# Performance work log

Measured on AMD Instinct MI355X. Metric: run time of the kernel, lower is better.

The kernel has to match this reference:

```python
import jax, jax.numpy as jnp
import numpy as np

B, T, C = 4, 2048, 1024
NH = 16
HD = C // NH


def setup_inputs() -> dict:
    key = jax.random.key(0)
    k1, k2, k3 = jax.random.split(key, 3)
    x = jax.random.normal(k1, (B, T, C), dtype=jnp.float32)
    Wqkv = jax.random.normal(k2, (C, 3 * C), dtype=jnp.float32) * 0.02
    bqkv = jnp.zeros((3 * C,), dtype=jnp.float32)
    Wproj = jax.random.normal(k3, (C, C), dtype=jnp.float32) * 0.02
    bproj = jnp.zeros((C,), dtype=jnp.float32)
    return {"x": x, "Wqkv": Wqkv, "bqkv": bqkv, "Wproj": Wproj, "bproj": bproj}


def reference(x, Wqkv, bqkv, Wproj, bproj):
    Bx, Tx, Cx = x.shape
    qkv = x @ Wqkv + bqkv  # [B,T,3C]
    q, k, v = jnp.split(qkv, 3, axis=-1)
    # [B, NH, T, HD]
    q = q.reshape(Bx, Tx, NH, HD).transpose(0, 2, 1, 3)
    k = k.reshape(Bx, Tx, NH, HD).transpose(0, 2, 1, 3)
    v = v.reshape(Bx, Tx, NH, HD).transpose(0, 2, 1, 3)
    scale = 1.0 / jnp.sqrt(jnp.float32(HD))
    att = jnp.einsum('bhqd,bhkd->bhqk', q, k) * scale  # [B,NH,T,T]
    causal = jnp.tril(jnp.ones((Tx, Tx), dtype=bool))
    att = jnp.where(causal, att, jnp.float32(-jnp.inf))
    att = jax.nn.softmax(att, axis=-1)
    y = jnp.einsum('bhqk,bhkd->bhqd', att, v)  # [B,NH,T,HD]
    y = y.transpose(0, 2, 1, 3).reshape(Bx, Tx, Cx)
    return y @ Wproj + bproj
```

## Files before the change

### kernel.cpp

```cpp
#include <hip/hip_runtime.h>
#include <hip/hip_bf16.h>
#include <math.h>

#define B_  4
#define T_  2048
#define C_  1024
#define NH_ 16
#define HD_ 64

using bf16 = __hip_bfloat16;
typedef __attribute__((ext_vector_type(8))) short bf16x8;
typedef __attribute__((ext_vector_type(4))) short bf16x4;
typedef __attribute__((ext_vector_type(4))) float f32x4;

__device__ __forceinline__ bf16 f2b(float f){ return __float2bfloat16(f); }

__device__ __forceinline__ short f2bs(float f){
  union { float f; unsigned u; } x; x.f = f;
  x.u += 0x7FFFu + ((x.u >> 16) & 1u);
  return (short)(x.u >> 16);
}

__device__ __forceinline__ bf16x4 pack_bf16x4(float a, float b, float c, float d){
  union { bf16x4 v; __hip_bfloat162 h[2]; } u;
  u.h[0] = __float22bfloat162_rn(make_float2(a, b));
  u.h[1] = __float22bfloat162_rn(make_float2(c, d));
  return u.v;
}

__device__ __forceinline__ float fexp2(float x){
  float r; asm("v_exp_f32 %0, %1" : "=v"(r) : "v"(x)); return r;
}

__device__ __forceinline__ void async_load16(const bf16* g, bf16* l){
  __builtin_amdgcn_global_load_lds((const __attribute__((address_space(1))) unsigned int*)g,
                                   (__attribute__((address_space(3))) unsigned int*)l,
                                   16, 0, 0);
}

#define QSCALE 0.18033688011112042f

__global__ __launch_bounds__(256) void k_prep(const float* __restrict__ x, bf16* __restrict__ xb, int n,
                                              const float* __restrict__ in0, bf16* __restrict__ out0,
                                              const float* __restrict__ in1, bf16* __restrict__ out1){
  __shared__ float t[32][33];
  int b = blockIdx.x;
  if (b < 8192){
    int i = (b * 256 + threadIdx.x) * 4;
    if (i < n){
      float4 f = *(const float4*)(x + i);
      ushort4 u;
      u.x = (unsigned short)f2bs(f.x);
      u.y = (unsigned short)f2bs(f.y);
      u.z = (unsigned short)f2bs(f.z);
      u.w = (unsigned short)f2bs(f.w);
      *(ushort4*)(xb + i) = u;
    }
    return;
  }
  b -= 8192;
  const float* in; bf16* out; int Cc, bx, by;
  if (b < 3072){ in = in0; out = out0; Cc = 3*C_; bx = (b % 96)*32; by = (b / 96)*32; }
  else { b -= 3072; in = in1; out = out1; Cc = C_; bx = (b & 31)*32; by = (b >> 5)*32; }
  const int R = C_;
  int lx = threadIdx.x & 31, ly = threadIdx.x >> 5;
  #pragma unroll
  for (int s = 0; s < 4; s++){
    int k = by + ly + s*8;
    t[ly + s*8][lx] = in[(size_t)k * Cc + bx + lx];
  }
  __syncthreads();
  #pragma unroll
  for (int s = 0; s < 4; s++){
    int n2 = bx + ly + s*8;
    out[(size_t)n2 * R + by + lx] = f2b(t[lx][ly + s*8]);
  }
}

__global__ __launch_bounds__(512) void k_gemm256(
    const bf16* __restrict__ A, const bf16* __restrict__ BT,
    const float* __restrict__ bias,
    bf16* __restrict__ qo, bf16* __restrict__ ko, bf16* __restrict__ vo,
    int M, int N, int K)
{
  extern __shared__ bf16 smem[];
  bf16* As = smem;
  bf16* Bs = smem + 4*8192;

  const int tid  = threadIdx.x;
  const int wave = tid >> 6, lane = tid & 63;
  const int wm = wave >> 2, wn = wave & 3;
  const int quad = lane >> 4, l15 = lane & 15;
  const int bm = blockIdx.x * 256;
  const int bn = blockIdx.y * 256;

  const bf16* gA[2]; const bf16* gB[2]; int lofs[2];
  #pragma unroll
  for (int s = 0; s < 2; s++){
    const int c = tid + s*512;
    const int r = c >> 2, p = (c & 3) ^ ((r >> 1) & 3);
    gA[s] = A  + (size_t)(bm + r)*K + p*8;
    gB[s] = BT + (size_t)(bn + r)*K + p*8;
    lofs[s] = c*8;
  }
  const int fsw = (l15 >> 1) & 3;

  f32x4 acc[8][4] = {};
  const int S = K >> 6;

  #pragma unroll
  for (int kh = 0; kh < 2; kh++){
    #pragma unroll
    for (int s = 0; s < 2; s++) async_load16(gA[s] + kh*32, As + kh*8192 + lofs[s]);
    #pragma unroll
    for (int s = 0; s < 2; s++) async_load16(gB[s] + kh*32, Bs + kh*8192 + lofs[s]);
  }

  for (int u = 0; u < S; u++){
    const int d  = u & 1;
    const int e2 = (d ^ 1) * 2;
    const bf16* a0 = As + (d*2+0)*8192;
    const bf16* a1 = As + (d*2+1)*8192;
    const bf16* b0 = Bs + (d*2+0)*8192;
    const bf16* b1 = Bs + (d*2+1)*8192;
    const bool pre = (u + 1 < S);
    const int off0 = (u + 1) * 64;

    bf16x8 bfv[4], af[4];

    asm volatile("s_waitcnt vmcnt(4)" ::: "memory");
    __builtin_amdgcn_s_barrier();
    __builtin_amdgcn_sched_barrier(0);
    if (pre){
      async_load16(gA[0] + off0, As + e2*8192 + lofs[0]);
      async_load16(gA[1] + off0, As + e2*8192 + lofs[1]);
    }
    #pragma unroll
    for (int j = 0; j < 4; j++)
      bfv[j] = *reinterpret_cast<const bf16x8*>(b0 + (wn*64 + j*16 + l15)*32 + ((quad ^ fsw) << 3));
    #pragma unroll
    for (int i = 0; i < 4; i++)
      af[i]  = *reinterpret_cast<const bf16x8*>(a0 + (wm*128 + i*16 + l15)*32 + ((quad ^ fsw) << 3));
    __builtin_amdgcn_s_setprio(1);
    #pragma unroll
    for (int i = 0; i < 4; i++)
      #pragma unroll
      for (int j = 0; j < 4; j++)
        acc[i][j] = __builtin_amdgcn_mfma_f32_16x16x32_bf16(af[i], bfv[j], acc[i][j], 0, 0, 0);
    __builtin_amdgcn_s_setprio(0);

    if (pre){
      async_load16(gB[0] + off0, Bs + e2*8192 + lofs[0]);
      async_load16(gB[1] + off0, Bs + e2*8192 + lofs[1]);
    }
    #pragma unroll
    for (int i = 0; i < 4; i++)
      af[i]  = *reinterpret_cast<const bf16x8*>(a0 + (wm*128 + 64 + i*16 + l15)*32 + ((quad ^ fsw) << 3));
    __builtin_amdgcn_s_setprio(1);
    #pragma unroll
    for (int i = 0; i < 4; i++)
      #pragma unroll
      for (int j = 0; j < 4; j++)
        acc[4+i][j] = __builtin_amdgcn_mfma_f32_16x16x32_bf16(af[i], bfv[j], acc[4+i][j], 0, 0, 0);
    __builtin_amdgcn_s_setprio(0);

    if (pre) asm volatile("s_waitcnt vmcnt(4)" ::: "memory");
    else     asm volatile("s_waitcnt vmcnt(0)" ::: "memory");
    __builtin_amdgcn_s_barrier();
    __builtin_amdgcn_sched_barrier(0);
    if (pre){
      async_load16(gA[0] + off0 + 32, As + (e2+1)*8192 + lofs[0]);
      async_load16(gA[1] + off0 + 32, As + (e2+1)*8192 + lofs[1]);
    }
    #pragma unroll
    for (int j = 0; j < 4; j++)
      bfv[j] = *reinterpret_cast<const bf16x8*>(b1 + (wn*64 + j*16 + l15)*32 + ((quad ^ fsw) << 3));
    #pragma unroll
    for (int i = 0; i < 4; i++)
      af[i]  = *reinterpret_cast<const bf16x8*>(a1 + (wm*128 + i*16 + l15)*32 + ((quad ^ fsw) << 3));
    __builtin_amdgcn_s_setprio(1);
    #pragma unroll
    for (int i = 0; i < 4; i++)
      #pragma unroll
      for (int j = 0; j < 4; j++)
        acc[i][j] = __builtin_amdgcn_mfma_f32_16x16x32_bf16(af[i], bfv[j], acc[i][j], 0, 0, 0);
    __builtin_amdgcn_s_setprio(0);

    if (pre){
      async_load16(gB[0] + off0 + 32, Bs + (e2+1)*8192 + lofs[0]);
      async_load16(gB[1] + off0 + 32, Bs + (e2+1)*8192 + lofs[1]);
    }
    #pragma unroll
    for (int i = 0; i < 4; i++)
      af[i]  = *reinterpret_cast<const bf16x8*>(a1 + (wm*128 + 64 + i*16 + l15)*32 + ((quad ^ fsw) << 3));
    __builtin_amdgcn_s_setprio(1);
    #pragma unroll
    for (int i = 0; i < 4; i++)
      #pragma unroll
      for (int j = 0; j < 4; j++)
        acc[4+i][j] = __builtin_amdgcn_mfma_f32_16x16x32_bf16(af[i], bfv[j], acc[4+i][j], 0, 0, 0);
    __builtin_amdgcn_s_setprio(0);
  }

  {
    const int sec = bn >> 10;
    const int bb2 = bm >> 11;
    const int tb  = (bm & (T_ - 1)) + wm*128 + quad*4;
    const int hn  = ((bn & 1023) >> 6) + wn;
    const size_t bhx = (size_t)(bb2 * NH_ + hn);
    if (sec == 2){
      #pragma unroll
      for (int j = 0; j < 4; j++){
        const int d2 = j*16 + l15;
        const float bj = bias[bn + wn*64 + j*16 + l15];
        bf16* vrow = vo + (bhx * HD_ + d2) * (size_t)T_;
        const int sw = (l15 & 7) * 8;
        #pragma unroll
        for (int i = 0; i < 8; i++){
          const int t = (tb + i*16) ^ sw;
          *reinterpret_cast<bf16x4*>(vrow + t) =
            pack_bf16x4(acc[i][j][0] + bj, acc[i][j][1] + bj,
                        acc[i][j][2] + bj, acc[i][j][3] + bj);
        }
      }
    } else {
      bf16* dst = (sec == 0) ? qo : ko;
      const float sc = (sec == 0) ? QSCALE : 1.0f;
      bf16* base = dst + bhx * T_ * HD_;
      float bj[4];
      #pragma unroll
      for (int j = 0; j < 4; j++) bj[j] = bias[bn + wn*64 + j*16 + l15];
      #pragma unroll
      for (int i = 0; i < 8; i++){
        #pragma unroll
        for (int r = 0; r < 4; r++){
          const int t  = tb + i*16 + r;
          const int sw2 = (t & 7) * 8;
          bf16* prow = base + (size_t)t * HD_;
          #pragma unroll
          for (int j = 0; j < 4; j++){
            const int dq = (j*16 + l15) ^ sw2;
            short s = f2bs((acc[i][j][r] + bj[j]) * sc);
            prow[dq] = *(bf16*)&s;
          }
        }
      }
    }
  }
}

template<int MODE>
__global__ __launch_bounds__(256, 2) void k_gemm8(
    const bf16* __restrict__ A, const bf16* __restrict__ BT,
    const float* __restrict__ bias,
    bf16* __restrict__ qo, bf16* __restrict__ ko, bf16* __restrict__ vo,
    float* __restrict__ fout,
    int M, int N, int K)
{
  __shared__ bf16 As[2][2][128*32];
  __shared__ bf16 Bs[2][2][128*32];

  const int tid  = threadIdx.x;
  const int wave = tid >> 6, lane = tid & 63;
  const int wm = wave & 1, wn = wave >> 1;
  const int quad = lane >> 4, l15 = lane & 15;
  const int bm = blockIdx.x * 128;
  const int bn = blockIdx.y * 128;

  const bf16* gA[2]; const bf16* gB[2]; int lofs[2];
  #pragma unroll
  for (int s = 0; s < 2; s++){
    const int c = tid + s*256;
    const int r = c >> 2, p = (c & 3) ^ ((r >> 1) & 3);
    gA[s] = A  + (size_t)(bm + r)*K + p*8;
    gB[s] = BT + (size_t)(bn + r)*K + p*8;
    lofs[s] = c*8;
  }
  const int fsw = (l15 >> 1) & 3;

  f32x4 acc[4][4] = {};
  const int nT = K >> 6;

  #pragma unroll
  for (int kh = 0; kh < 2; kh++)
    #pragma unroll
    for (int s = 0; s < 2; s++){
      async_load16(gA[s] + kh*32, &As[0][kh][0] + lofs[s]);
      async_load16(gB[s] + kh*32, &Bs[0][kh][0] + lofs[s]);
    }

  for (int u = 0; u < nT; u++){
    const int d = u & 1;
    #pragma unroll
    for (int kh = 0; kh < 2; kh++){
      if (u + 1 < nT || kh == 0) asm volatile("s_waitcnt vmcnt(4)" ::: "memory");
      else                       asm volatile("s_waitcnt vmcnt(0)" ::: "memory");
      __builtin_amdgcn_s_barrier();
      __builtin_amdgcn_sched_barrier(0);

      const bf16* as = &As[d][kh][0];
      const bf16* bs = &Bs[d][kh][0];
      bf16x8 af[4], bfv[4];
      #pragma unroll
      for (int i = 0; i < 4; i++)
        af[i]  = *reinterpret_cast<const bf16x8*>(as + (wm*64 + i*16 + l15)*32 + ((quad ^ fsw) << 3));
      #pragma unroll
      for (int j = 0; j < 4; j++)
        bfv[j] = *reinterpret_cast<const bf16x8*>(bs + (wn*64 + j*16 + l15)*32 + ((quad ^ fsw) << 3));

      if (u + 1 < nT){
        const int ko2 = (u + 1)*64 + kh*32;
        #pragma unroll
        for (int s = 0; s < 2; s++){
          async_load16(gA[s] + ko2, &As[d^1][kh][0] + lofs[s]);
          async_load16(gB[s] + ko2, &Bs[d^1][kh][0] + lofs[s]);
        }
      }

      __builtin_amdgcn_s_setprio(1);
      #pragma unroll
      for (int i = 0; i < 4; i++)
        #pragma unroll
        for (int j = 0; j < 4; j++)
          acc[i][j] = __builtin_amdgcn_mfma_f32_16x16x32_bf16(af[i], bfv[j], acc[i][j], 0, 0, 0);
      __builtin_amdgcn_s_setprio(0);
    }
  }

  if (MODE == 0){
    const int sec = bn >> 10;
    const int bb2 = bm >> 11;
    const int tb  = (bm & (T_ - 1)) + wm*64 + quad*4;
    const int hn  = ((bn & 1023) >> 6) + wn;
    const size_t bhx = (size_t)(bb2 * NH_ + hn);
    if (sec == 2){
      #pragma unroll
      for (int j = 0; j < 4; j++){
        const int d2 = j*16 + l15;
        const float bj = bias[bn + wn*64 + j*16 + l15];
        bf16* vrow = vo + (bhx * HD_ + d2) * (size_t)T_;
        const int sw = (l15 & 7) * 8;
        #pragma unroll
        for (int i = 0; i < 4; i++){
          const int t = (tb + i*16) ^ sw;
          *reinterpret_cast<bf16x4*>(vrow + t) =
            pack_bf16x4(acc[i][j][0] + bj, acc[i][j][1] + bj,
                        acc[i][j][2] + bj, acc[i][j][3] + bj);
        }
      }
    } else {
      bf16* dst = (sec == 0) ? qo : ko;
      const float sc = (sec == 0) ? QSCALE : 1.0f;
      bf16* base = dst + bhx * T_ * HD_;
      float bj[4];
      #pragma unroll
      for (int j = 0; j < 4; j++) bj[j] = bias[bn + wn*64 + j*16 + l15];
      #pragma unroll
      for (int i = 0; i < 4; i++){
        #pragma unroll
        for (int r = 0; r < 4; r++){
          const int t  = tb + i*16 + r;
          const int sw2 = (t & 7) * 8;
          bf16* prow = base + (size_t)t * HD_;
          #pragma unroll
          for (int j = 0; j < 4; j++){
            const int dq = (j*16 + l15) ^ sw2;
            short s = f2bs((acc[i][j][r] + bj[j]) * sc);
            prow[dq] = *(bf16*)&s;
          }
        }
      }
    }
  } else {
    const int n0 = bn + wn*64 + l15;
    float bj[4];
    #pragma unroll
    for (int j = 0; j < 4; j++) bj[j] = bias[n0 + j*16];
    #pragma unroll
    for (int i = 0; i < 4; i++){
      #pragma unroll
      for (int r = 0; r < 4; r++){
        float* p0 = fout + (size_t)(bm + wm*64 + i*16 + quad*4 + r) * N + n0;
        #pragma unroll
        for (int j = 0; j < 4; j++)
          p0[j*16] = acc[i][j][r] + bj[j];
      }
    }
  }
}

__global__ __launch_bounds__(256) void k_attn(
    const bf16* __restrict__ Q, const bf16* __restrict__ Kg,
    const bf16* __restrict__ Vt, bf16* __restrict__ Y)
{
  __shared__ bf16 Ks[2][64*64];
  __shared__ bf16 Vs[2][64*64];

  const int bh = blockIdx.x;
  const int bb = bh >> 4, hh = bh & 15;
  const int qt = 15 - blockIdx.y;
  const int tid  = threadIdx.x;
  const int wave = tid >> 6, lane = tid & 63;
  const int quad = lane >> 4, l15 = lane & 15;
  const int swz  = (l15 & 7) * 8;

  const size_t baseQK = (size_t)bh * T_ * HD_;
  const size_t baseV  = (size_t)bh * HD_ * T_;

  const int ca = wave, cb = wave + 4;
  const bf16* kg_a = Kg + baseQK + ca*512 + (size_t)lane*8;
  const bf16* kg_b = Kg + baseQK + cb*512 + (size_t)lane*8;
  const bf16* vg_a = Vt + baseV + (size_t)(ca*8 + (lane>>3)) * T_ + (lane&7)*8;
  const bf16* vg_b = Vt + baseV + (size_t)(cb*8 + (lane>>3)) * T_ + (lane&7)*8;
  bf16* kl_a0 = &Ks[0][0] + ca*512;  bf16* kl_b0 = &Ks[0][0] + cb*512;
  bf16* vl_a0 = &Vs[0][0] + ca*512;  bf16* vl_b0 = &Vs[0][0] + cb*512;

  bf16x4 ones_f;
  {
    short v = (l15 == 0) ? f2bs(1.0f) : (short)0;
    ones_f = (bf16x4){ v, v, v, v };
  }
  const f32x4 ZV = {0.0f, 0.0f, 0.0f, 0.0f};

  bf16x8 qf[2][2];
  #pragma unroll
  for (int s = 0; s < 2; s++){
    const int t = qt*128 + s*64 + wave*16 + l15;
    #pragma unroll
    for (int ks = 0; ks < 2; ks++){
      const int col = (ks*32 + quad*8) ^ swz;
      qf[s][ks] = *reinterpret_cast<const bf16x8*>(Q + baseQK + (size_t)t*HD_ + col);
    }
  }

  async_load16(kg_a, kl_a0);  async_load16(kg_b, kl_b0);
  async_load16(vg_a, vl_a0);  async_load16(vg_b, vl_b0);

  f32x4 o[2][5] = {};

  for (int j = 0; j <= 2*qt; j++){
    __syncthreads();

    {
      const int nb = ((j+1) & 1) * 4096;
      const size_t ko = (size_t)(j+1) * 64 * HD_;
      async_load16(kg_a + ko, kl_a0 + nb);  async_load16(kg_b + ko, kl_b0 + nb);
      async_load16(vg_a + (j+1)*64, vl_a0 + nb);
      async_load16(vg_b + (j+1)*64, vl_b0 + nb);
    }

    const bf16* ksb = &Ks[j & 1][0];
    const bf16* vsb = &Vs[j & 1][0];

    f32x4 st[2][4];
    __builtin_amdgcn_s_setprio(1);
    #pragma unroll
    for (int tk = 0; tk < 4; tk++){
      bf16x8 kf0 = *reinterpret_cast<const bf16x8*>(ksb + (tk*16 + l15)*64 + ((quad*8) ^ swz));
      bf16x8 kf1 = *reinterpret_cast<const bf16x8*>(ksb + (tk*16 + l15)*64 + ((32 + quad*8) ^ swz));
      st[0][tk] = __builtin_amdgcn_mfma_f32_16x16x32_bf16(kf0, qf[0][0], ZV, 0, 0, 0);
      st[1][tk] = __builtin_amdgcn_mfma_f32_16x16x32_bf16(kf0, qf[1][0], ZV, 0, 0, 0);
      st[0][tk] = __builtin_amdgcn_mfma_f32_16x16x32_bf16(kf1, qf[0][1], st[0][tk], 0, 0, 0);
      st[1][tk] = __builtin_amdgcn_mfma_f32_16x16x32_bf16(kf1, qf[1][1], st[1][tk], 0, 0, 0);
    }
    __builtin_amdgcn_s_setprio(0);

    bf16x4 pf[2][4];
    {
      const int qg = qt*128 + wave*16 + l15;
      const bool msk = (j == 2*qt);
      #pragma unroll
      for (int tk = 0; tk < 4; tk++){
        float e[4];
        #pragma unroll
        for (int r = 0; r < 4; r++){
          float sv = st[0][tk][r];
          if (msk){
            const int kvg = j*64 + tk*16 + quad*4 + r;
            if (kvg > qg) sv = -1e30f;
          }
          e[r] = fexp2(sv);
        }
        pf[0][tk] = pack_bf16x4(e[0], e[1], e[2], e[3]);
      }
    }
    #pragma unroll
    for (int tk = 0; tk < 4; tk++){
      float e[4];
      #pragma unroll
      for (int r = 0; r < 4; r++) e[r] = fexp2(st[1][tk][r]);
      pf[1][tk] = pack_bf16x4(e[0], e[1], e[2], e[3]);
    }

    __builtin_amdgcn_s_setprio(1);
    #pragma unroll
    for (int td = 0; td < 4; td++){
      #pragma unroll
      for (int tk = 0; tk < 4; tk++){
        bf16x4 vf = *reinterpret_cast<const bf16x4*>(vsb + (td*16 + l15)*64 + ((tk*16 + quad*4) ^ swz));
        o[0][td] = __builtin_amdgcn_mfma_f32_16x16x16bf16_1k(vf, pf[0][tk], o[0][td], 0, 0, 0);
        o[1][td] = __builtin_amdgcn_mfma_f32_16x16x16bf16_1k(vf, pf[1][tk], o[1][td], 0, 0, 0);
      }
    }
    #pragma unroll
    for (int tk = 0; tk < 4; tk++){
      o[0][4] = __builtin_amdgcn_mfma_f32_16x16x16bf16_1k(ones_f, pf[0][tk], o[0][4], 0, 0, 0);
      o[1][4] = __builtin_amdgcn_mfma_f32_16x16x16bf16_1k(ones_f, pf[1][tk], o[1][4], 0, 0, 0);
    }
    __builtin_amdgcn_s_setprio(0);
  }

  {
    const int j = 2*qt + 1;
    __syncthreads();

    const bf16* ksb = &Ks[j & 1][0];
    const bf16* vsb = &Vs[j & 1][0];

    f32x4 st1[4];
    __builtin_amdgcn_s_setprio(1);
    #pragma unroll
    for (int tk = 0; tk < 4; tk++){
      bf16x8 kf0 = *reinterpret_cast<const bf16x8*>(ksb + (tk*16 + l15)*64 + ((quad*8) ^ swz));
      bf16x8 kf1 = *reinterpret_cast<const bf16x8*>(ksb + (tk*16 + l15)*64 + ((32 + quad*8) ^ swz));
      st1[tk] = __builtin_amdgcn_mfma_f32_16x16x32_bf16(kf0, qf[1][0], ZV, 0, 0, 0);
      st1[tk] = __builtin_amdgcn_mfma_f32_16x16x32_bf16(kf1, qf[1][1], st1[tk], 0, 0, 0);
    }
    __builtin_amdgcn_s_setprio(0);

    bf16x4 pf1[4];
    {
      const int qg = qt*128 + 64 + wave*16 + l15;
      #pragma unroll
      for (int tk = 0; tk < 4; tk++){
        float e[4];
        #pragma unroll
        for (int r = 0; r < 4; r++){
          float sv = st1[tk][r];
          const int kvg = j*64 + tk*16 + quad*4 + r;
          if (kvg > qg) sv = -1e30f;
          e[r] = fexp2(sv);
        }
        pf1[tk] = pack_bf16x4(e[0], e[1], e[2], e[3]);
      }
    }

    __builtin_amdgcn_s_setprio(1);
    #pragma unroll
    for (int td = 0; td < 4; td++){
      #pragma unroll
      for (int tk = 0; tk < 4; tk++){
        bf16x4 vf = *reinterpret_cast<const bf16x4*>(vsb + (td*16 + l15)*64 + ((tk*16 + quad*4) ^ swz));
        o[1][td] = __builtin_amdgcn_mfma_f32_16x16x16bf16_1k(vf, pf1[tk], o[1][td], 0, 0, 0);
      }
    }
    #pragma unroll
    for (int tk = 0; tk < 4; tk++)
      o[1][4] = __builtin_amdgcn_mfma_f32_16x16x16bf16_1k(ones_f, pf1[tk], o[1][4], 0, 0, 0);
    __builtin_amdgcn_s_setprio(0);
  }

  #pragma unroll
  for (int s = 0; s < 2; s++){
    const float l = __shfl(o[s][4][0], l15, 64);
    const float inv = 1.0f / l;
    const int t = qt*128 + s*64 + wave*16 + l15;
    bf16* yrow = Y + ((size_t)(bb * T_ + t)) * C_ + hh * HD_;
    #pragma unroll
    for (int td = 0; td < 4; td++){
      *reinterpret_cast<bf16x4*>(yrow + td*16 + quad*4) =
        pack_bf16x4(o[s][td][0] * inv, o[s][td][1] * inv,
                    o[s][td][2] * inv, o[s][td][3] * inv);
    }
  }
}


extern "C" void kernel_launch(void* const* d_in, const int* in_sizes, int n_in,
                              void* d_out, int out_size, void* d_ws, size_t ws_size,
                              hipStream_t stream) {
  const float* x     = (const float*)d_in[0];
  const float* Wqkv  = (const float*)d_in[1];
  const float* bqkv  = (const float*)d_in[2];
  const float* Wproj = (const float*)d_in[3];
  const float* bproj = (const float*)d_in[4];
  float* out = (float*)d_out;

  const size_t M = (size_t)B_ * T_;
  char* w = (char*)d_ws;
  bf16* xb     = (bf16*)w;  w += M * C_ * 2;
  bf16* WqkvT  = (bf16*)w;  w += (size_t)3 * C_ * C_ * 2;
  bf16* WprojT = (bf16*)w;  w += (size_t)C_ * C_ * 2;
  bf16* Qb     = (bf16*)w;  w += M * C_ * 2;
  bf16* Kb     = (bf16*)w;  w += M * C_ * 2;
  bf16* Vtb    = (bf16*)w;  w += M * C_ * 2;
  bf16* Yb     = (bf16*)w;  w += M * C_ * 2;

  static bool attr_done = false;
  if (!attr_done){
    hipFuncSetAttribute(reinterpret_cast<const void*>(k_gemm256),
                        hipFuncAttributeMaxDynamicSharedMemorySize, 131072);
    attr_done = true;
  }

  {
    int n = (int)(M * C_);
    k_prep<<<dim3(12288), dim3(256), 0, stream>>>(x, xb, n, Wqkv, WqkvT, Wproj, WprojT);
  }
  k_gemm256<<<dim3(M/256, (3*C_)/256), dim3(512), 131072, stream>>>(
      xb, WqkvT, bqkv, Qb, Kb, Vtb, (int)M, 3*C_, C_);
  k_attn<<<dim3(64, 16), dim3(256), 0, stream>>>(Qb, Kb, Vtb, Yb);
  k_gemm8<1><<<dim3(M/128, C_/128), dim3(256), 0, stream>>>(
      Yb, WprojT, bproj, nullptr, nullptr, nullptr, out, (int)M, C_, C_);
}
```

Before: 232.1 us.

## Restructure QKV GEMM mainloop to one barrier per step with batched prefetch

The main loop of the 256x256 QKV GEMM drops from two barriers per K-step to one. It waits for all outstanding loads (vmcnt(0)), then issues all eight async prefetches for the next stage together, and uses separate register fragments so LDS reads interleave with the MFMA blocks. Launch bounds now request two blocks of 512 threads per CU. The aim is less barrier and sync overhead and more latency hiding through occupancy. The risks are register spills under the tighter bound and a weaker load/compute overlap, since the wait now drains everything.

```diff
diff --git a/kernel.cpp b/kernel.cpp
--- a/kernel.cpp
+++ b/kernel.cpp
@@ -77,7 +77,7 @@
   }
 }
 
-__global__ __launch_bounds__(512) void k_gemm256(
+__global__ __launch_bounds__(512, 2) void k_gemm256(
     const bf16* __restrict__ A, const bf16* __restrict__ BT,
     const float* __restrict__ bias,
     bf16* __restrict__ qo, bf16* __restrict__ ko, bf16* __restrict__ vo,
@@ -126,79 +126,73 @@
     const bool pre = (u + 1 < S);
     const int off0 = (u + 1) * 64;
 
-    bf16x8 bfv[4], af[4];
-
-    asm volatile("s_waitcnt vmcnt(4)" ::: "memory");
+    asm volatile("s_waitcnt vmcnt(0)" ::: "memory");
     __builtin_amdgcn_s_barrier();
     __builtin_amdgcn_sched_barrier(0);
+
+    bf16x8 bfv0[4], bfv1[4], afA[4], afB[4];
+
+    #pragma unroll
+    for (int j = 0; j < 4; j++)
+      bfv0[j] = *reinterpret_cast<const bf16x8*>(b0 + (wn*64 + j*16 + l15)*32 + ((quad ^ fsw) << 3));
+    #pragma unroll
+    for (int i = 0; i < 4; i++)
+      afA[i]  = *reinterpret_cast<const bf16x8*>(a0 + (wm*128 + i*16 + l15)*32 + ((quad ^ fsw) << 3));
+
     if (pre){
-      async_load16(gA[0] + off0, As + e2*8192 + lofs[0]);
-      async_load16(gA[1] + off0, As + e2*8192 + lofs[1]);
-    }
-    #pragma unroll
-    for (int j = 0; j < 4; j++)
-      bfv[j] = *reinterpret_cast<const bf16x8*>(b0 + (wn*64 + j*16 + l15)*32 + ((quad ^ fsw) << 3));
-    #pragma unroll
-    for (int i = 0; i < 4; i++)
-      af[i]  = *reinterpret_cast<const bf16x8*>(a0 + (wm*128 + i*16 + l15)*32 + ((quad ^ fsw) << 3));
-    __builtin_amdgcn_s_setprio(1);
-    #pragma unroll
-    for (int i = 0; i < 4; i++)
-      #pragma unroll
-      for (int j = 0; j < 4; j++)
-        acc[i][j] = __builtin_amdgcn_mfma_f32_16x16x32_bf16(af[i], bfv[j], acc[i][j], 0, 0, 0);
-    __builtin_amdgcn_s_setprio(0);
-
-    if (pre){
-      async_load16(gB[0] + off0, Bs + e2*8192 + lofs[0]);
-      async_load16(gB[1] + off0, Bs + e2*8192 + lofs[1]);
-    }
-    #pragma unroll
-    for (int i = 0; i < 4; i++)
-      af[i]  = *reinterpret_cast<const bf16x8*>(a0 + (wm*128 + 64 + i*16 + l15)*32 + ((quad ^ fsw) << 3));
-    __builtin_amdgcn_s_setprio(1);
-    #pragma unroll
-    for (int i = 0; i < 4; i++)
-      #pragma unroll
-      for (int j = 0; j < 4; j++)
-        acc[4+i][j] = __builtin_amdgcn_mfma_f32_16x16x32_bf16(af[i], bfv[j], acc[4+i][j], 0, 0, 0);
-    __builtin_amdgcn_s_setprio(0);
-
-    if (pre) asm volatile("s_waitcnt vmcnt(4)" ::: "memory");
-    else     asm volatile("s_waitcnt vmcnt(0)" ::: "memory");
-    __builtin_amdgcn_s_barrier();
-    __builtin_amdgcn_sched_barrier(0);
-    if (pre){
+      async_load16(gA[0] + off0,      As + e2*8192 + lofs[0]);
+      async_load16(gA[1] + off0,      As + e2*8192 + lofs[1]);
+      async_load16(gB[0] + off0,      Bs + e2*8192 + lofs[0]);
+      async_load16(gB[1] + off0,      Bs + e2*8192 + lofs[1]);
       async_load16(gA[0] + off0 + 32, As + (e2+1)*8192 + lofs[0]);
       async_load16(gA[1] + off0 + 32, As + (e2+1)*8192 + lofs[1]);
-    }
-    #pragma unroll
-    for (int j = 0; j < 4; j++)
-      bfv[j] = *reinterpret_cast<const bf16x8*>(b1 + (wn*64 + j*16 + l15)*32 + ((quad ^ fsw) << 3));
-    #pragma unroll
-    for (int i = 0; i < 4; i++)
-      af[i]  = *reinterpret_cast<const bf16x8*>(a1 + (wm*128 + i*16 + l15)*32 + ((quad ^ fsw) << 3));
-    __builtin_amdgcn_s_setprio(1);
-    #pragma unroll
-    for (int i = 0; i < 4; i++)
-      #pragma unroll
-      for (int j = 0; j < 4; j++)
-        acc[i][j] = __builtin_amdgcn_mfma_f32_16x16x32_bf16(af[i], bfv[j], acc[i][j], 0, 0, 0);
-    __builtin_amdgcn_s_setprio(0);
-
-    if (pre){
       async_load16(gB[0] + off0 + 32, Bs + (e2+1)*8192 + lofs[0]);
       async_load16(gB[1] + off0 + 32, Bs + (e2+1)*8192 + lofs[1]);
     }
-    #pragma unroll
-    for (int i = 0; i < 4; i++)
-      af[i]  = *reinterpret_cast<const bf16x8*>(a1 + (wm*128 + 64 + i*16 + l15)*32 + ((quad ^ fsw) << 3));
+
+    #pragma unroll
+    for (int i = 0; i < 4; i++)
+      afB[i]  = *reinterpret_cast<const bf16x8*>(a0 + (wm*128 + 64 + i*16 + l15)*32 + ((quad ^ fsw) << 3));
+
     __builtin_amdgcn_s_setprio(1);
     #pragma unroll
     for (int i = 0; i < 4; i++)
       #pragma unroll
       for (int j = 0; j < 4; j++)
-        acc[4+i][j] = __builtin_amdgcn_mfma_f32_16x16x32_bf16(af[i], bfv[j], acc[4+i][j], 0, 0, 0);
+        acc[i][j] = __builtin_amdgcn_mfma_f32_16x16x32_bf16(afA[i], bfv0[j], acc[i][j], 0, 0, 0);
+    __builtin_amdgcn_s_setprio(0);
+
+    #pragma unroll
+    for (int j = 0; j < 4; j++)
+      bfv1[j] = *reinterpret_cast<const bf16x8*>(b1 + (wn*64 + j*16 + l15)*32 + ((quad ^ fsw) << 3));
+    #pragma unroll
+    for (int i = 0; i < 4; i++)
+      afA[i]  = *reinterpret_cast<const bf16x8*>(a1 + (wm*128 + i*16 + l15)*32 + ((quad ^ fsw) << 3));
+
+    __builtin_amdgcn_s_setprio(1);
+    #pragma unroll
+    for (int i = 0; i < 4; i++)
+      #pragma unroll
+      for (int j = 0; j < 4; j++)
+        acc[4+i][j] = __builtin_amdgcn_mfma_f32_16x16x32_bf16(afB[i], bfv0[j], acc[4+i][j], 0, 0, 0);
+    __builtin_amdgcn_s_setprio(0);
+
+    #pragma unroll
+    for (int i = 0; i < 4; i++)
+      afB[i]  = *reinterpret_cast<const bf16x8*>(a1 + (wm*128 + 64 + i*16 + l15)*32 + ((quad ^ fsw) << 3));
+
+    __builtin_amdgcn_s_setprio(1);
+    #pragma unroll
+    for (int i = 0; i < 4; i++)
+      #pragma unroll
+      for (int j = 0; j < 4; j++)
+        acc[i][j] = __builtin_amdgcn_mfma_f32_16x16x32_bf16(afA[i], bfv1[j], acc[i][j], 0, 0, 0);
+
+    #pragma unroll
+    for (int i = 0; i < 4; i++)
+      #pragma unroll
+      for (int j = 0; j < 4; j++)
+        acc[4+i][j] = __builtin_amdgcn_mfma_f32_16x16x32_bf16(afB[i], bfv1[j], acc[4+i][j], 0, 0, 0);
     __builtin_amdgcn_s_setprio(0);
   }
 
```

Result: slower. 237.6 us (+2.4%).
